# Optimization experiments

Hardware: AMD Instinct MI355X
Metric: run time of the kernel (lower is better)

## Reference

```python
import jax, jax.numpy as jnp
import numpy as np

EPS = 1e-12
ATTEND_SCALE = 8.0

def _l2norm(t, axis=-1):
    n = jnp.sqrt(jnp.sum(t * t, axis=axis, keepdims=True))
    return t / jnp.maximum(n, EPS)

def setup_inputs() -> dict:
    key = jax.random.key(0)
    k1, k2, k3, k4 = jax.random.split(key, 4)
    b, n, dim = 4, 8192, 1024
    heads, dim_head = 16, 64
    dim_inner = heads * dim_head
    x = jax.random.normal(k1, (b, n, dim), dtype=jnp.float32)
    gamma = jnp.ones((dim,), dtype=jnp.float32)  # RMSNorm gamma
    # torch Linear(dim, 3*dim_inner, bias=False): store as [dim, 3*dim_inner] for x @ W
    w_qkv = jax.random.normal(k2, (dim, 3 * dim_inner), dtype=jnp.float32) * (dim ** -0.5)
    temperature = jnp.zeros((heads, 1, 1), dtype=jnp.float32)
    w_out = jax.random.normal(k3, (dim_inner, dim), dtype=jnp.float32) * (dim_inner ** -0.5)
    return {"x": x, "gamma": gamma, "w_qkv": w_qkv, "temperature": temperature, "w_out": w_out}

def reference(x, gamma, w_qkv, temperature, w_out):
    b, n, dim = x.shape
    heads = temperature.shape[0]
    dim_head = w_qkv.shape[1] // (3 * heads)
    # RMSNorm: F.normalize(x, dim=-1) * sqrt(dim) * gamma
    xn = _l2norm(x) * (dim ** 0.5) * gamma
    qkv = xn @ w_qkv  # [b, n, 3*h*d]
    qkv = qkv.reshape(b, n, 3, heads, dim_head).transpose(2, 0, 3, 4, 1)  # [3, b, h, d, n]
    q, k, v = qkv[0], qkv[1], qkv[2]
    orig_v = v
    # l2-normalize q, k over the sequence axis (last dim of [b,h,d,n])
    q = _l2norm(q) * jnp.exp(temperature)  # temperature [h,1,1] broadcasts
    k = _l2norm(k)
    # attention over the feature axis: sim [b, h, d, d]
    sim = jnp.einsum('bhdn,bhen->bhde', q, k) * ATTEND_SCALE
    attn = jax.nn.softmax(sim, axis=-1)
    out = jnp.einsum('bhde,bhen->bhdn', attn, v)  # [b, h, d, n]
    out = out.transpose(0, 3, 1, 2).reshape(b, n, heads * dim_head) @ w_out  # [b, n, dim]
    return out, orig_v
```

## Files before the change

### kernel.cpp

```cpp
#include <hip/hip_runtime.h>
#include <hip/hip_bf16.h>

#define DEVI __device__ __forceinline__

using bf16x8 = __attribute__((ext_vector_type(8))) __bf16;
using f32x4  = __attribute__((ext_vector_type(4))) float;
using u16x8  = __attribute__((ext_vector_type(8))) unsigned short;

DEVI unsigned short f2bf(float f) {
  unsigned int u = __float_as_uint(f);
  u = (u + 0x7FFFu + ((u >> 16) & 1u)) >> 16;
  return (unsigned short)u;
}
DEVI float bf2f(unsigned short s) { return __uint_as_float(((unsigned int)s) << 16); }

DEVI void gld_lds16(const unsigned short* g, unsigned short* l) {
  __builtin_amdgcn_global_load_lds(
      (const __attribute__((address_space(1))) void*)g,
      (__attribute__((address_space(3))) void*)l, 16, 0, 0);
}

__global__ __launch_bounds__(256) void transpose_cast_kernel(const float* __restrict__ in,
                                                             unsigned short* __restrict__ out,
                                                             int R, int C) {
  __shared__ float tile[32][33];
  const int c0 = blockIdx.x * 32, r0 = blockIdx.y * 32;
  const int tx = threadIdx.x & 31, ty = threadIdx.x >> 5;
  for (int rr = ty; rr < 32; rr += 8)
    tile[rr][tx] = in[(size_t)(r0 + rr) * C + c0 + tx];
  __syncthreads();
  for (int cc = ty; cc < 32; cc += 8)
    out[(size_t)(c0 + cc) * R + r0 + tx] = f2bf(tile[tx][cc]);
}

__global__ __launch_bounds__(256) void castv_kernel(const float* __restrict__ w_qkv,
                                                    unsigned short* __restrict__ Wv_nt) {
  const int i = blockIdx.x * 256 + threadIdx.x;
  const int k = i >> 8, he4 = (i & 255) * 4;
  const float4 v = *(const float4*)&w_qkv[(size_t)k * 3072 + 2048 + he4];
  ushort4 o;
  o.x = f2bf(v.x); o.y = f2bf(v.y); o.z = f2bf(v.z); o.w = f2bf(v.w);
  *(ushort4*)&Wv_nt[(size_t)k * 1024 + he4] = o;
}

__global__ __launch_bounds__(256) void transpose_bf16x4_kernel(const unsigned short* __restrict__ in,
                                                               unsigned short* __restrict__ out) {
  __shared__ unsigned short tile[64][68];
  const int r0 = blockIdx.x * 64;
  const int c0 = blockIdx.y * 64;
  const int t = threadIdx.x;
  const int tr = t >> 4, tc4 = (t & 15) * 4;
#pragma unroll
  for (int p = 0; p < 4; ++p) {
    const int rr = p * 16 + tr;
    *(ushort4*)&tile[rr][tc4] = *(const ushort4*)&in[(size_t)(r0 + rr) * 1024 + c0 + tc4];
  }
  __syncthreads();
#pragma unroll
  for (int p = 0; p < 4; ++p) {
    const int cc = p * 16 + tr;
    ushort4 o;
    o.x = tile[tc4 + 0][cc];
    o.y = tile[tc4 + 1][cc];
    o.z = tile[tc4 + 2][cc];
    o.w = tile[tc4 + 3][cc];
    *(ushort4*)&out[(size_t)(c0 + cc) * 32768 + r0 + tc4] = o;
  }
}

__global__ __launch_bounds__(256) void rmsnorm_kernel(const float* __restrict__ x,
                                                      const float* __restrict__ gamma,
                                                      unsigned short* __restrict__ xn) {
  __shared__ float wsum[4];
  const int row = blockIdx.x;
  const int t = threadIdx.x;
  const float4 v = *(const float4*)&x[(size_t)row * 1024 + t * 4];
  float s = v.x * v.x + v.y * v.y + v.z * v.z + v.w * v.w;
  for (int off = 32; off; off >>= 1) s += __shfl_down(s, off);
  if ((t & 63) == 0) wsum[t >> 6] = s;
  __syncthreads();
  const float tot = wsum[0] + wsum[1] + wsum[2] + wsum[3];
  const float scale = 32.0f / fmaxf(sqrtf(tot), 1e-12f);
  const float4 g = *(const float4*)&gamma[t * 4];
  ushort4 o;
  o.x = f2bf(v.x * scale * g.x);
  o.y = f2bf(v.y * scale * g.y);
  o.z = f2bf(v.z * scale * g.z);
  o.w = f2bf(v.w * scale * g.w);
  *(ushort4*)&xn[(size_t)row * 1024 + t * 4] = o;
}

__global__ __launch_bounds__(256) void gemm_gram_kernel(const unsigned short* __restrict__ xnT,
                                                        unsigned short* __restrict__ Gp) {
  if (blockIdx.x > blockIdx.y) return;
  __shared__ __align__(16) unsigned short Al[4096];
  __shared__ __align__(16) unsigned short Bl[4096];
  const int tid = threadIdx.x;
  const int lane = tid & 63, wid = tid >> 6;
  const int wr = wid >> 1, wc = wid & 1;
  const int r = lane & 15, kg = lane >> 4;
  const int rw0 = tid >> 2, q0 = (tid & 3) * 8;
  const size_t row0 = (size_t)blockIdx.y * 128, col0 = (size_t)blockIdx.x * 128;
  const int z = blockIdx.z;
  const size_t koff = (size_t)(z >> 2) * 8192 + (size_t)(z & 3) * 2048;
  f32x4 acc[4][4] = {};
  for (int k0 = 0; k0 < 2048; k0 += 32) {
    __syncthreads();
    gld_lds16(&xnT[(row0 + rw0) * 32768 + koff + k0 + q0], &Al[tid * 8]);
    gld_lds16(&xnT[(row0 + rw0 + 64) * 32768 + koff + k0 + q0], &Al[2048 + tid * 8]);
    gld_lds16(&xnT[(col0 + rw0) * 32768 + koff + k0 + q0], &Bl[tid * 8]);
    gld_lds16(&xnT[(col0 + rw0 + 64) * 32768 + koff + k0 + q0], &Bl[2048 + tid * 8]);
    __syncthreads();
    bf16x8 af[4], bfr[4];
#pragma unroll
    for (int m = 0; m < 4; ++m) af[m] = *(const bf16x8*)&Al[(wr * 64 + m * 16 + r) * 32 + kg * 8];
#pragma unroll
    for (int n = 0; n < 4; ++n) bfr[n] = *(const bf16x8*)&Bl[(wc * 64 + n * 16 + r) * 32 + kg * 8];
#pragma unroll
    for (int m = 0; m < 4; ++m)
#pragma unroll
      for (int n = 0; n < 4; ++n)
        acc[m][n] = __builtin_amdgcn_mfma_f32_16x16x32_bf16(af[m], bfr[n], acc[m][n], 0, 0, 0);
  }
  unsigned short* C = Gp + ((size_t)z << 20);
  const int rbase = wr * 64 + (lane >> 4) * 4;
  const int cbase = wc * 64 + (lane & 15);
#pragma unroll
  for (int m = 0; m < 4; ++m)
#pragma unroll
    for (int n = 0; n < 4; ++n)
#pragma unroll
      for (int j = 0; j < 4; ++j)
        C[(row0 + rbase + m * 16 + j) * 1024 + col0 + cbase + n * 16] = f2bf(acc[m][n][j]);
}

__global__ __launch_bounds__(256) void greduce_kernel(const unsigned short* __restrict__ Gp,
                                                      unsigned short* __restrict__ G) {
  const int tj = blockIdx.x, ti = blockIdx.y, b = blockIdx.z;
  if ((tj >> 1) > (ti >> 1)) return;
  __shared__ float lds[64][65];
  const int t = threadIdx.x;
  const int r = t >> 2, c0 = (t & 3) * 16;
  const size_t idx = (size_t)(ti * 64 + r) * 1024 + tj * 64 + c0;
  float v[16];
#pragma unroll
  for (int j = 0; j < 16; ++j) v[j] = 0.f;
  for (int s = 0; s < 4; ++s) {
    const unsigned short* p = Gp + ((size_t)(b * 4 + s) << 20) + idx;
#pragma unroll
    for (int j = 0; j < 16; ++j) v[j] += bf2f(p[j]);
  }
  unsigned short* Gb = G + ((size_t)b << 20);
  __attribute__((aligned(16))) unsigned short buf[16];
#pragma unroll
  for (int j = 0; j < 16; ++j) buf[j] = f2bf(v[j]);
  { int4* dst = (int4*)&Gb[idx]; const int4* src = (const int4*)buf; dst[0] = src[0]; dst[1] = src[1]; }
  if ((ti >> 1) != (tj >> 1)) {
#pragma unroll
    for (int j = 0; j < 16; ++j) lds[r][c0 + j] = v[j];
    __syncthreads();
    const int x = t >> 2, y0 = (t & 3) * 16;
#pragma unroll
    for (int j = 0; j < 16; ++j) buf[j] = f2bf(lds[y0 + j][x]);
    int4* dst = (int4*)&Gb[(size_t)(tj * 64 + x) * 1024 + ti * 64 + y0];
    const int4* src = (const int4*)buf;
    dst[0] = src[0]; dst[1] = src[1];
  }
}

__global__ __launch_bounds__(256) void gemm_bt_batch_bf16(const unsigned short* __restrict__ A,
                                                          const unsigned short* __restrict__ Bt,
                                                          unsigned short* __restrict__ C,
                                                          int N, int K,
                                                          long long aStr, long long bStr, long long cStr) {
  __shared__ __align__(16) unsigned short Al[4096];
  __shared__ __align__(16) unsigned short Bl[4096];
  A += (size_t)blockIdx.z * aStr; Bt += (size_t)blockIdx.z * bStr; C += (size_t)blockIdx.z * cStr;
  const int tid = threadIdx.x;
  const int lane = tid & 63, wid = tid >> 6;
  const int wr = wid >> 1, wc = wid & 1;
  const int r = lane & 15, kg = lane >> 4;
  const int rw0 = tid >> 2, q0 = (tid & 3) * 8;
  const size_t row0 = (size_t)blockIdx.y * 128, col0 = (size_t)blockIdx.x * 128;
  f32x4 acc[4][4] = {};
  for (int k0 = 0; k0 < K; k0 += 32) {
    __syncthreads();
    gld_lds16(&A[(row0 + rw0) * K + k0 + q0], &Al[tid * 8]);
    gld_lds16(&A[(row0 + rw0 + 64) * K + k0 + q0], &Al[2048 + tid * 8]);
    gld_lds16(&Bt[(col0 + rw0) * K + k0 + q0], &Bl[tid * 8]);
    gld_lds16(&Bt[(col0 + rw0 + 64) * K + k0 + q0], &Bl[2048 + tid * 8]);
    __syncthreads();
    bf16x8 af[4], bfr[4];
#pragma unroll
    for (int m = 0; m < 4; ++m) af[m] = *(const bf16x8*)&Al[(wr * 64 + m * 16 + r) * 32 + kg * 8];
#pragma unroll
    for (int n = 0; n < 4; ++n) bfr[n] = *(const bf16x8*)&Bl[(wc * 64 + n * 16 + r) * 32 + kg * 8];
#pragma unroll
    for (int m = 0; m < 4; ++m)
#pragma unroll
      for (int n = 0; n < 4; ++n)
        acc[m][n] = __builtin_amdgcn_mfma_f32_16x16x32_bf16(af[m], bfr[n], acc[m][n], 0, 0, 0);
  }
  const int rbase = wr * 64 + (lane >> 4) * 4;
  const int cbase = wc * 64 + (lane & 15);
#pragma unroll
  for (int m = 0; m < 4; ++m)
#pragma unroll
    for (int n = 0; n < 4; ++n)
#pragma unroll
      for (int j = 0; j < 4; ++j)
        C[(row0 + rbase + m * 16 + j) * N + col0 + cbase + n * 16] = f2bf(acc[m][n][j]);
}

DEVI void stage256(const unsigned short* __restrict__ gA,
                   const unsigned short* __restrict__ gB,
                   unsigned short* lA, unsigned short* lB,
                   int k0, int w, int lane) {
  const int dr = lane >> 3;
  const int ks = (lane & 7) ^ dr;
  const size_t lo = (size_t)dr * 1024 + k0 + ks * 8;
#pragma unroll
  for (int i = 0; i < 4; ++i) {
    const int oct = w * 4 + i;
    gld_lds16(gA + (size_t)oct * 8192 + lo, lA + oct * 512 + lane * 8);
    gld_lds16(gB + (size_t)oct * 8192 + lo, lB + oct * 512 + lane * 8);
  }
}

DEVI void compute256(const unsigned short* __restrict__ lA,
                     const unsigned short* __restrict__ lB,
                     int wm, int wn, int lane, f32x4 (&acc)[8][4]) {
  const int r = lane & 15, kg = lane >> 4;
  const int r7 = r & 7;
#pragma unroll
  for (int ksl = 0; ksl < 2; ++ksl) {
    const int sA = (((ksl << 2) + kg) ^ r7) * 8;
    bf16x8 af[8], bfr[4];
#pragma unroll
    for (int m = 0; m < 8; ++m)
      af[m] = *(const bf16x8*)&lA[(wm * 128 + m * 16 + r) * 64 + sA];
#pragma unroll
    for (int n = 0; n < 4; ++n)
      bfr[n] = *(const bf16x8*)&lB[(wn * 64 + n * 16 + r) * 64 + sA];
#pragma unroll
    for (int m = 0; m < 8; ++m)
#pragma unroll
      for (int n = 0; n < 4; ++n)
        acc[m][n] = __builtin_amdgcn_mfma_f32_16x16x32_bf16(af[m], bfr[n], acc[m][n], 0, 0, 0);
  }
}

#define VOUT_BAR()  __builtin_amdgcn_sched_barrier(0); __builtin_amdgcn_s_barrier(); \
                    __builtin_amdgcn_sched_barrier(0)
#define VOUT_W8()   asm volatile("s_waitcnt vmcnt(8)" ::: "memory")
#define VOUT_W0()   asm volatile("s_waitcnt vmcnt(0)" ::: "memory")

__global__ __launch_bounds__(512, 2) void gemm_vout256_kernel(
    const unsigned short* __restrict__ A,
    const unsigned short* __restrict__ BtV,
    const unsigned short* __restrict__ WfoldT,
    float* __restrict__ origv,
    float* __restrict__ outp) {
  __shared__ __align__(16) unsigned short Al[2][16384];
  __shared__ __align__(16) unsigned short Bl[2][16384];
  const int tid = threadIdx.x;
  const int lane = tid & 63;
  const int w = tid >> 6;
  const int wm = w >> 2, wn = w & 3;
  const int cb = blockIdx.x & 7;
  const int rb = blockIdx.x >> 3;
  const int b = rb >> 5;
  const unsigned short* gA = A + (size_t)rb * 256 * 1024;
  const unsigned short* gB = (cb < 4)
      ? BtV + (size_t)cb * 256 * 1024
      : WfoldT + ((size_t)b << 20) + (size_t)(cb - 4) * 256 * 1024;

  f32x4 acc[8][4] = {};
  stage256(gA, gB, Al[0], Bl[0], 0, w, lane);
#pragma unroll 1
  for (int tt = 0; tt < 7; ++tt) {
    stage256(gA, gB, Al[1], Bl[1], (tt * 2 + 1) * 64, w, lane);
    VOUT_W8(); VOUT_BAR();
    __builtin_amdgcn_s_setprio(1);
    compute256(Al[0], Bl[0], wm, wn, lane, acc);
    __builtin_amdgcn_s_setprio(0);
    VOUT_BAR();
    stage256(gA, gB, Al[0], Bl[0], (tt * 2 + 2) * 64, w, lane);
    VOUT_W8(); VOUT_BAR();
    __builtin_amdgcn_s_setprio(1);
    compute256(Al[1], Bl[1], wm, wn, lane, acc);
    __builtin_amdgcn_s_setprio(0);
    VOUT_BAR();
  }
  stage256(gA, gB, Al[1], Bl[1], 15 * 64, w, lane);
  VOUT_W8(); VOUT_BAR();
  __builtin_amdgcn_s_setprio(1);
  compute256(Al[0], Bl[0], wm, wn, lane, acc);
  __builtin_amdgcn_s_setprio(0);
  VOUT_BAR();
  VOUT_W0(); VOUT_BAR();
  __builtin_amdgcn_s_setprio(1);
  compute256(Al[1], Bl[1], wm, wn, lane, acc);
  __builtin_amdgcn_s_setprio(0);

  const int rr = (lane >> 4) * 4;
  const int cc = lane & 15;
  if (cb < 4) {
    const int nbase = (rb & 31) * 256 + wm * 128;
#pragma unroll
    for (int m = 0; m < 8; ++m)
#pragma unroll
      for (int n = 0; n < 4; ++n) {
        const int hd = cb * 256 + wn * 64 + n * 16 + cc;
        const float4 o4 = make_float4(acc[m][n][0], acc[m][n][1], acc[m][n][2], acc[m][n][3]);
        *(float4*)&origv[((size_t)b * 1024 + hd) * 8192 + nbase + m * 16 + rr] = o4;
      }
  } else {
    const size_t grow0 = (size_t)rb * 256 + wm * 128;
    const int gc0 = (cb - 4) * 256 + wn * 64;
#pragma unroll
    for (int m = 0; m < 8; ++m)
#pragma unroll
      for (int n = 0; n < 4; ++n)
#pragma unroll
        for (int j = 0; j < 4; ++j)
          outp[(grow0 + m * 16 + rr + j) * 1024 + gc0 + n * 16 + cc] = acc[m][n][j];
  }
}

__global__ __launch_bounds__(256) void norms_kernel(const unsigned short* __restrict__ UTt,
                                                    const unsigned short* __restrict__ wqkvT,
                                                    float* __restrict__ qkn2) {
  const int t = threadIdx.x;
  const int rloc = t >> 4, lane16 = t & 15;
  const int row = blockIdx.x * 16 + rloc;
  const int b = row >> 11, r2 = row & 2047;
  const unsigned short* pa = UTt + ((size_t)b << 21) + (size_t)r2 * 1024 + lane16 * 64;
  const unsigned short* pb = wqkvT + (size_t)r2 * 1024 + lane16 * 64;
  float s = 0.f;
  for (int i = 0; i < 64; i += 8) {
    const u16x8 va = *(const u16x8*)&pa[i];
    const u16x8 vb = *(const u16x8*)&pb[i];
#pragma unroll
    for (int j = 0; j < 8; ++j) s += bf2f(va[j]) * bf2f(vb[j]);
  }
  for (int off = 8; off; off >>= 1) s += __shfl_down(s, off, 16);
  if (lane16 == 0) qkn2[row] = s;
}

__global__ __launch_bounds__(256) void sim_softmax_kernel(const unsigned short* __restrict__ wqkvT,
                                                          const unsigned short* __restrict__ UTt,
                                                          const float* __restrict__ qkn2,
                                                          const float* __restrict__ temperature,
                                                          float* __restrict__ attn) {
  __shared__ __align__(16) unsigned short Aql[64 * 128];
  __shared__ __align__(16) unsigned short Bkl[64 * 128];
  __shared__ float qknl[2][64];
  const int bh = blockIdx.x;
  const int b = bh >> 4, h = bh & 15;
  const int t = threadIdx.x;
  const int lane = t & 63, w = t >> 6;
  const unsigned short* UTtb = UTt + ((size_t)b << 21);
  if (t < 128) {
    const int sel = t >> 6, dd = t & 63;
    qknl[sel][dd] = fmaxf(sqrtf(qkn2[b * 2048 + sel * 1024 + h * 64 + dd]), 1e-12f);
  }
  const unsigned short* AqG = UTtb + (size_t)(h * 64) * 1024;
  const unsigned short* BkG = wqkvT + (size_t)(1024 + h * 64) * 1024;
  const int r = lane & 15, kg = lane >> 4;
  const int srow = t >> 4, scol = (t & 15) * 8;
  f32x4 acc[4] = {};
  for (int k0 = 0; k0 < 1024; k0 += 128) {
    __syncthreads();
#pragma unroll
    for (int c = 0; c < 4; ++c) {
      gld_lds16(&AqG[(size_t)(c * 16 + srow) * 1024 + k0 + scol], &Aql[c * 2048 + t * 8]);
      gld_lds16(&BkG[(size_t)(c * 16 + srow) * 1024 + k0 + scol], &Bkl[c * 2048 + t * 8]);
    }
    __syncthreads();
#pragma unroll
    for (int kk = 0; kk < 128; kk += 32) {
      const bf16x8 af = *(const bf16x8*)&Aql[(w * 16 + r) * 128 + kk + kg * 8];
#pragma unroll
      for (int n = 0; n < 4; ++n) {
        const bf16x8 bfr = *(const bf16x8*)&Bkl[(n * 16 + r) * 128 + kk + kg * 8];
        acc[n] = __builtin_amdgcn_mfma_f32_16x16x32_bf16(af, bfr, acc[n], 0, 0, 0);
      }
    }
  }
  const float sc = 8.f * __expf(temperature[h]);
  const int colq = lane & 15, rq = lane >> 4;
#pragma unroll
  for (int j = 0; j < 4; ++j) {
    const int d = w * 16 + rq * 4 + j;
    const float qd = qknl[0][d];
    float sv[4];
#pragma unroll
    for (int n = 0; n < 4; ++n) sv[n] = acc[n][j] * sc / (qd * qknl[1][n * 16 + colq]);
    float mj = fmaxf(fmaxf(sv[0], sv[1]), fmaxf(sv[2], sv[3]));
    for (int msk = 1; msk < 16; msk <<= 1) mj = fmaxf(mj, __shfl_xor(mj, msk));
    float p[4], sum = 0.f;
#pragma unroll
    for (int n = 0; n < 4; ++n) { p[n] = __expf(sv[n] - mj); sum += p[n]; }
    for (int msk = 1; msk < 16; msk <<= 1) sum += __shfl_xor(sum, msk);
    const float inv = 1.f / sum;
#pragma unroll
    for (int n = 0; n < 4; ++n)
      attn[(size_t)bh * 4096 + d * 64 + n * 16 + colq] = p[n] * inv;
  }
}

__global__ __launch_bounds__(256) void w2t_kernel(const float* __restrict__ attn,
                                                  const float* __restrict__ w_out,
                                                  unsigned short* __restrict__ W2T) {
  __shared__ float al[64][64];
  __shared__ float wl[64][64];
  const int bh = blockIdx.y;
  const int b = bh >> 4, h = bh & 15;
  const int c0 = blockIdx.x * 256;
  const int t = threadIdx.x, e = t & 63, g = t >> 6;
  const int dr = t >> 2, q4 = (t & 3) * 16;
#pragma unroll
  for (int j = 0; j < 16; j += 4)
    *(float4*)&al[dr][q4 + j] = *(const float4*)&attn[(size_t)bh * 4096 + dr * 64 + q4 + j];
  for (int cbk = 0; cbk < 4; ++cbk) {
    __syncthreads();
#pragma unroll
    for (int j = 0; j < 16; j += 4)
      *(float4*)&wl[dr][q4 + j] = *(const float4*)&w_out[(size_t)(h * 64 + dr) * 1024 + c0 + cbk * 64 + q4 + j];
    __syncthreads();
#pragma unroll
    for (int i = 0; i < 16; ++i) {
      const int cc = g * 16 + i;
      float s = 0.f;
#pragma unroll 8
      for (int d = 0; d < 64; ++d) s += al[d][e] * wl[d][cc];
      W2T[((size_t)b << 20) + (size_t)(c0 + cbk * 64 + cc) * 1024 + h * 64 + e] = f2bf(s);
    }
  }
}

extern "C" void kernel_launch(void* const* d_in, const int* in_sizes, int n_in,
                              void* d_out, int out_size, void* d_ws, size_t ws_size,
                              hipStream_t stream) {
  const float* x     = (const float*)d_in[0];
  const float* gamma = (const float*)d_in[1];
  const float* w_qkv = (const float*)d_in[2];
  const float* temp  = (const float*)d_in[3];
  const float* w_out = (const float*)d_in[4];
  char* ws = (char*)d_ws;
  unsigned short* wqkvT  = (unsigned short*)(ws);
  unsigned short* Wv_nt  = (unsigned short*)(ws + 6291456);
  unsigned short* xn     = (unsigned short*)(ws + 8388608);
  unsigned short* xnT    = (unsigned short*)(ws + 75497472);
  unsigned short* Gp     = (unsigned short*)(ws + 142606336);
  unsigned short* G      = (unsigned short*)(ws + 176160768);
  unsigned short* UTt    = (unsigned short*)(ws + 184549376);
  float* qkn2            = (float*)(ws + 201326592);
  float* attn            = (float*)(ws + 201359360);
  unsigned short* W2T    = (unsigned short*)(ws + 202407936);
  unsigned short* WfoldT = (unsigned short*)(ws + 210796544);
  float* outp  = (float*)d_out;
  float* origv = outp + (size_t)33554432;

  transpose_cast_kernel<<<dim3(96, 32), 256, 0, stream>>>(w_qkv, wqkvT, 1024, 3072);
  castv_kernel<<<1024, 256, 0, stream>>>(w_qkv, Wv_nt);
  rmsnorm_kernel<<<32768, 256, 0, stream>>>(x, gamma, xn);
  transpose_bf16x4_kernel<<<dim3(512, 16), 256, 0, stream>>>(xn, xnT);
  gemm_gram_kernel<<<dim3(8, 8, 16), 256, 0, stream>>>(xnT, Gp);
  greduce_kernel<<<dim3(16, 16, 4), 256, 0, stream>>>(Gp, G);
  gemm_bt_batch_bf16<<<dim3(8, 16, 4), 256, 0, stream>>>(wqkvT, G, UTt, 1024, 1024,
                                                         0LL, 1LL << 20, 1LL << 21);
  norms_kernel<<<512, 256, 0, stream>>>(UTt, wqkvT, qkn2);
  sim_softmax_kernel<<<64, 256, 0, stream>>>(wqkvT, UTt, qkn2, temp, attn);
  w2t_kernel<<<dim3(4, 64), 256, 0, stream>>>(attn, w_out, W2T);
  gemm_bt_batch_bf16<<<dim3(8, 8, 4), 256, 0, stream>>>(W2T, Wv_nt, WfoldT, 1024, 1024,
                                                        1LL << 20, 0LL, 1LL << 20);
  gemm_vout256_kernel<<<1024, 512, 0, stream>>>(xn, wqkvT + (size_t)2048 * 1024, WfoldT,
                                                origv, outp);
}
```

Measured before the change: 510.8 us.

## Restructure vout GEMM into 4-slot K=32 pipeline with three slices in flight

Replaces the double-buffered K=64 staging in the fused V/out GEMM with a 4-slot ring of K=32 slices, keeping three global-to-LDS loads in flight while one slice is computed. The LDS swizzle changes to match the narrower 32-element rows, and the barriers drop the compiler sched_barrier fences in favour of plain asm s_barrier. The aim is to hide more global-load latency behind the MFMAs. In exchange it needs twice as many barriers per K step, gives the compiler less to schedule per barrier, and the swizzle has only four positions, which may cause more LDS bank conflicts.

```diff
diff --git a/kernel.cpp b/kernel.cpp
--- a/kernel.cpp
+++ b/kernel.cpp
@@ -212,48 +212,48 @@
         C[(row0 + rbase + m * 16 + j) * N + col0 + cbase + n * 16] = f2bf(acc[m][n][j]);
 }
 
-DEVI void stage256(const unsigned short* __restrict__ gA,
-                   const unsigned short* __restrict__ gB,
-                   unsigned short* lA, unsigned short* lB,
-                   int k0, int w, int lane) {
-  const int dr = lane >> 3;
-  const int ks = (lane & 7) ^ dr;
-  const size_t lo = (size_t)dr * 1024 + k0 + ks * 8;
-#pragma unroll
-  for (int i = 0; i < 4; ++i) {
-    const int oct = w * 4 + i;
-    gld_lds16(gA + (size_t)oct * 8192 + lo, lA + oct * 512 + lane * 8);
-    gld_lds16(gB + (size_t)oct * 8192 + lo, lB + oct * 512 + lane * 8);
-  }
-}
-
-DEVI void compute256(const unsigned short* __restrict__ lA,
-                     const unsigned short* __restrict__ lB,
-                     int wm, int wn, int lane, f32x4 (&acc)[8][4]) {
+DEVI void stage_slice(const unsigned short* __restrict__ gA,
+                      const unsigned short* __restrict__ gB,
+                      unsigned short* lA, unsigned short* lB,
+                      int s, int slot, int w, int lane) {
+  const int ric = lane >> 2;
+  const int phys = lane & 3;
+  const int kg = phys ^ (ric & 3);
+#pragma unroll
+  for (int i = 0; i < 2; ++i) {
+    const int c = w * 2 + i;
+    const int row = c * 16 + ric;
+    const size_t goff = (size_t)row * 1024 + s * 32 + kg * 8;
+    gld_lds16(gA + goff, lA + slot * 8192 + c * 512 + lane * 8);
+    gld_lds16(gB + goff, lB + slot * 8192 + c * 512 + lane * 8);
+  }
+}
+
+DEVI void compute_slice(const unsigned short* lA, const unsigned short* lB,
+                        int slot, int wm, int wn, int lane, f32x4 (&acc)[8][4]) {
   const int r = lane & 15, kg = lane >> 4;
-  const int r7 = r & 7;
-#pragma unroll
-  for (int ksl = 0; ksl < 2; ++ksl) {
-    const int sA = (((ksl << 2) + kg) ^ r7) * 8;
-    bf16x8 af[8], bfr[4];
-#pragma unroll
-    for (int m = 0; m < 8; ++m)
-      af[m] = *(const bf16x8*)&lA[(wm * 128 + m * 16 + r) * 64 + sA];
+  const int sA = (kg ^ (r & 3)) * 8;
+  const unsigned short* pA = lA + slot * 8192 + (wm * 128 + r) * 32 + sA;
+  const unsigned short* pB = lB + slot * 8192 + (wn * 64 + r) * 32 + sA;
+  bf16x8 af[8], bfr[4];
+#pragma unroll
+  for (int m = 0; m < 8; ++m) af[m] = *(const bf16x8*)(pA + m * 512);
+#pragma unroll
+  for (int n = 0; n < 4; ++n) bfr[n] = *(const bf16x8*)(pB + n * 512);
+  __builtin_amdgcn_s_setprio(1);
+#pragma unroll
+  for (int m = 0; m < 8; ++m)
 #pragma unroll
     for (int n = 0; n < 4; ++n)
-      bfr[n] = *(const bf16x8*)&lB[(wn * 64 + n * 16 + r) * 64 + sA];
-#pragma unroll
-    for (int m = 0; m < 8; ++m)
-#pragma unroll
-      for (int n = 0; n < 4; ++n)
-        acc[m][n] = __builtin_amdgcn_mfma_f32_16x16x32_bf16(af[m], bfr[n], acc[m][n], 0, 0, 0);
-  }
-}
-
-#define VOUT_BAR()  __builtin_amdgcn_sched_barrier(0); __builtin_amdgcn_s_barrier(); \
-                    __builtin_amdgcn_sched_barrier(0)
-#define VOUT_W8()   asm volatile("s_waitcnt vmcnt(8)" ::: "memory")
-#define VOUT_W0()   asm volatile("s_waitcnt vmcnt(0)" ::: "memory")
+      acc[m][n] = __builtin_amdgcn_mfma_f32_16x16x32_bf16(af[m], bfr[n], acc[m][n], 0, 0, 0);
+  __builtin_amdgcn_s_setprio(0);
+}
+
+#define VBAR()  asm volatile("s_barrier" ::: "memory")
+#define VW12()  asm volatile("s_waitcnt vmcnt(12)" ::: "memory")
+#define VW8()   asm volatile("s_waitcnt vmcnt(8)" ::: "memory")
+#define VW4()   asm volatile("s_waitcnt vmcnt(4)" ::: "memory")
+#define VW0()   asm volatile("s_waitcnt vmcnt(0)" ::: "memory")
 
 __global__ __launch_bounds__(512, 2) void gemm_vout256_kernel(
     const unsigned short* __restrict__ A,
@@ -261,8 +261,8 @@
     const unsigned short* __restrict__ WfoldT,
     float* __restrict__ origv,
     float* __restrict__ outp) {
-  __shared__ __align__(16) unsigned short Al[2][16384];
-  __shared__ __align__(16) unsigned short Bl[2][16384];
+  __shared__ __align__(16) unsigned short lA[4 * 8192];
+  __shared__ __align__(16) unsigned short lB[4 * 8192];
   const int tid = threadIdx.x;
   const int lane = tid & 63;
   const int w = tid >> 6;
@@ -276,32 +276,25 @@
       : WfoldT + ((size_t)b << 20) + (size_t)(cb - 4) * 256 * 1024;
 
   f32x4 acc[8][4] = {};
-  stage256(gA, gB, Al[0], Bl[0], 0, w, lane);
+  stage_slice(gA, gB, lA, lB, 0, 0, w, lane);
+  stage_slice(gA, gB, lA, lB, 1, 1, w, lane);
+  stage_slice(gA, gB, lA, lB, 2, 2, w, lane);
 #pragma unroll 1
-  for (int tt = 0; tt < 7; ++tt) {
-    stage256(gA, gB, Al[1], Bl[1], (tt * 2 + 1) * 64, w, lane);
-    VOUT_W8(); VOUT_BAR();
-    __builtin_amdgcn_s_setprio(1);
-    compute256(Al[0], Bl[0], wm, wn, lane, acc);
-    __builtin_amdgcn_s_setprio(0);
-    VOUT_BAR();
-    stage256(gA, gB, Al[0], Bl[0], (tt * 2 + 2) * 64, w, lane);
-    VOUT_W8(); VOUT_BAR();
-    __builtin_amdgcn_s_setprio(1);
-    compute256(Al[1], Bl[1], wm, wn, lane, acc);
-    __builtin_amdgcn_s_setprio(0);
-    VOUT_BAR();
-  }
-  stage256(gA, gB, Al[1], Bl[1], 15 * 64, w, lane);
-  VOUT_W8(); VOUT_BAR();
-  __builtin_amdgcn_s_setprio(1);
-  compute256(Al[0], Bl[0], wm, wn, lane, acc);
-  __builtin_amdgcn_s_setprio(0);
-  VOUT_BAR();
-  VOUT_W0(); VOUT_BAR();
-  __builtin_amdgcn_s_setprio(1);
-  compute256(Al[1], Bl[1], wm, wn, lane, acc);
-  __builtin_amdgcn_s_setprio(0);
+  for (int t4 = 0; t4 < 7; ++t4) {
+    const int sb = t4 * 4;
+#pragma unroll
+    for (int j = 0; j < 4; ++j) {
+      stage_slice(gA, gB, lA, lB, sb + j + 3, (j + 3) & 3, w, lane);
+      VW12(); VBAR();
+      compute_slice(lA, lB, j, wm, wn, lane, acc);
+      VBAR();
+    }
+  }
+  stage_slice(gA, gB, lA, lB, 31, 3, w, lane);
+  VW12(); VBAR(); compute_slice(lA, lB, 0, wm, wn, lane, acc); VBAR();
+  VW8();  VBAR(); compute_slice(lA, lB, 1, wm, wn, lane, acc); VBAR();
+  VW4();  VBAR(); compute_slice(lA, lB, 2, wm, wn, lane, acc); VBAR();
+  VW0();  VBAR(); compute_slice(lA, lB, 3, wm, wn, lane, acc);
 
   const int rr = (lane >> 4) * 4;
   const int cc = lane & 15;
```

Result: slower. 523.3 us (+2.4%).

## Use 256x256 double-buffered MFMA tiles for the Gram GEMM

Applied to the files above, without the earlier changes.

Replaces the 128x128 single-buffered Gram kernel with a 512-thread, 256x256-tile kernel. It reuses the swizzled, double-buffered global-to-LDS staging and compute helpers from the vout GEMM, with their staging stride now a parameter. The aim is higher data reuse per LDS load and overlap of loads with MFMA work. The reduction kernel's lower-triangle tile test is adjusted to the coarser block granularity. The catch is fewer blocks (4x4 triangle x16, so 160 active) on a large GPU, which may underfill the compute units.

```diff
diff --git a/kernel.cpp b/kernel.cpp
--- a/kernel.cpp
+++ b/kernel.cpp
@@ -90,54 +90,109 @@
   *(ushort4*)&xn[(size_t)row * 1024 + t * 4] = o;
 }
 
-__global__ __launch_bounds__(256) void gemm_gram_kernel(const unsigned short* __restrict__ xnT,
-                                                        unsigned short* __restrict__ Gp) {
+DEVI void stage256(const unsigned short* __restrict__ gA,
+                   const unsigned short* __restrict__ gB,
+                   unsigned short* lA, unsigned short* lB,
+                   int k0, int w, int lane, size_t gstride) {
+  const int dr = lane >> 3;
+  const int ks = (lane & 7) ^ dr;
+  const size_t lo = (size_t)dr * gstride + k0 + ks * 8;
+#pragma unroll
+  for (int i = 0; i < 4; ++i) {
+    const int oct = w * 4 + i;
+    gld_lds16(gA + (size_t)oct * 8 * gstride + lo, lA + oct * 512 + lane * 8);
+    gld_lds16(gB + (size_t)oct * 8 * gstride + lo, lB + oct * 512 + lane * 8);
+  }
+}
+
+DEVI void compute256(const unsigned short* __restrict__ lA,
+                     const unsigned short* __restrict__ lB,
+                     int wm, int wn, int lane, f32x4 (&acc)[8][4]) {
+  const int r = lane & 15, kg = lane >> 4;
+  const int r7 = r & 7;
+#pragma unroll
+  for (int ksl = 0; ksl < 2; ++ksl) {
+    const int sA = (((ksl << 2) + kg) ^ r7) * 8;
+    bf16x8 af[8], bfr[4];
+#pragma unroll
+    for (int m = 0; m < 8; ++m)
+      af[m] = *(const bf16x8*)&lA[(wm * 128 + m * 16 + r) * 64 + sA];
+#pragma unroll
+    for (int n = 0; n < 4; ++n)
+      bfr[n] = *(const bf16x8*)&lB[(wn * 64 + n * 16 + r) * 64 + sA];
+#pragma unroll
+    for (int m = 0; m < 8; ++m)
+#pragma unroll
+      for (int n = 0; n < 4; ++n)
+        acc[m][n] = __builtin_amdgcn_mfma_f32_16x16x32_bf16(af[m], bfr[n], acc[m][n], 0, 0, 0);
+  }
+}
+
+#define VOUT_BAR()  __builtin_amdgcn_sched_barrier(0); __builtin_amdgcn_s_barrier(); \
+                    __builtin_amdgcn_sched_barrier(0)
+#define VOUT_W8()   asm volatile("s_waitcnt vmcnt(8)" ::: "memory")
+#define VOUT_W0()   asm volatile("s_waitcnt vmcnt(0)" ::: "memory")
+
+__global__ __launch_bounds__(512, 2) void gemm_gram256_kernel(
+    const unsigned short* __restrict__ xnT, unsigned short* __restrict__ Gp) {
   if (blockIdx.x > blockIdx.y) return;
-  __shared__ __align__(16) unsigned short Al[4096];
-  __shared__ __align__(16) unsigned short Bl[4096];
+  __shared__ __align__(16) unsigned short Al[2][16384];
+  __shared__ __align__(16) unsigned short Bl[2][16384];
   const int tid = threadIdx.x;
-  const int lane = tid & 63, wid = tid >> 6;
-  const int wr = wid >> 1, wc = wid & 1;
-  const int r = lane & 15, kg = lane >> 4;
-  const int rw0 = tid >> 2, q0 = (tid & 3) * 8;
-  const size_t row0 = (size_t)blockIdx.y * 128, col0 = (size_t)blockIdx.x * 128;
+  const int lane = tid & 63;
+  const int w = tid >> 6;
+  const int wm = w >> 2, wn = w & 3;
   const int z = blockIdx.z;
   const size_t koff = (size_t)(z >> 2) * 8192 + (size_t)(z & 3) * 2048;
-  f32x4 acc[4][4] = {};
-  for (int k0 = 0; k0 < 2048; k0 += 32) {
-    __syncthreads();
-    gld_lds16(&xnT[(row0 + rw0) * 32768 + koff + k0 + q0], &Al[tid * 8]);
-    gld_lds16(&xnT[(row0 + rw0 + 64) * 32768 + koff + k0 + q0], &Al[2048 + tid * 8]);
-    gld_lds16(&xnT[(col0 + rw0) * 32768 + koff + k0 + q0], &Bl[tid * 8]);
-    gld_lds16(&xnT[(col0 + rw0 + 64) * 32768 + koff + k0 + q0], &Bl[2048 + tid * 8]);
-    __syncthreads();
-    bf16x8 af[4], bfr[4];
-#pragma unroll
-    for (int m = 0; m < 4; ++m) af[m] = *(const bf16x8*)&Al[(wr * 64 + m * 16 + r) * 32 + kg * 8];
-#pragma unroll
-    for (int n = 0; n < 4; ++n) bfr[n] = *(const bf16x8*)&Bl[(wc * 64 + n * 16 + r) * 32 + kg * 8];
-#pragma unroll
-    for (int m = 0; m < 4; ++m)
-#pragma unroll
-      for (int n = 0; n < 4; ++n)
-        acc[m][n] = __builtin_amdgcn_mfma_f32_16x16x32_bf16(af[m], bfr[n], acc[m][n], 0, 0, 0);
-  }
+  const unsigned short* gA = xnT + (size_t)blockIdx.y * 256 * 32768 + koff;
+  const unsigned short* gB = xnT + (size_t)blockIdx.x * 256 * 32768 + koff;
+
+  f32x4 acc[8][4] = {};
+  stage256(gA, gB, Al[0], Bl[0], 0, w, lane, 32768);
+#pragma unroll 1
+  for (int tt = 0; tt < 15; ++tt) {
+    stage256(gA, gB, Al[1], Bl[1], (tt * 2 + 1) * 64, w, lane, 32768);
+    VOUT_W8(); VOUT_BAR();
+    __builtin_amdgcn_s_setprio(1);
+    compute256(Al[0], Bl[0], wm, wn, lane, acc);
+    __builtin_amdgcn_s_setprio(0);
+    VOUT_BAR();
+    stage256(gA, gB, Al[0], Bl[0], (tt * 2 + 2) * 64, w, lane, 32768);
+    VOUT_W8(); VOUT_BAR();
+    __builtin_amdgcn_s_setprio(1);
+    compute256(Al[1], Bl[1], wm, wn, lane, acc);
+    __builtin_amdgcn_s_setprio(0);
+    VOUT_BAR();
+  }
+  stage256(gA, gB, Al[1], Bl[1], 31 * 64, w, lane, 32768);
+  VOUT_W8(); VOUT_BAR();
+  __builtin_amdgcn_s_setprio(1);
+  compute256(Al[0], Bl[0], wm, wn, lane, acc);
+  __builtin_amdgcn_s_setprio(0);
+  VOUT_BAR();
+  VOUT_W0(); VOUT_BAR();
+  __builtin_amdgcn_s_setprio(1);
+  compute256(Al[1], Bl[1], wm, wn, lane, acc);
+  __builtin_amdgcn_s_setprio(0);
+
   unsigned short* C = Gp + ((size_t)z << 20);
-  const int rbase = wr * 64 + (lane >> 4) * 4;
-  const int cbase = wc * 64 + (lane & 15);
-#pragma unroll
-  for (int m = 0; m < 4; ++m)
+  const int rr = (lane >> 4) * 4;
+  const int cc = lane & 15;
+  const size_t grow0 = (size_t)blockIdx.y * 256 + wm * 128;
+  const int gc0 = blockIdx.x * 256 + wn * 64;
+#pragma unroll
+  for (int m = 0; m < 8; ++m)
 #pragma unroll
     for (int n = 0; n < 4; ++n)
 #pragma unroll
       for (int j = 0; j < 4; ++j)
-        C[(row0 + rbase + m * 16 + j) * 1024 + col0 + cbase + n * 16] = f2bf(acc[m][n][j]);
+        C[(grow0 + m * 16 + rr + j) * 1024 + gc0 + n * 16 + cc] = f2bf(acc[m][n][j]);
 }
 
 __global__ __launch_bounds__(256) void greduce_kernel(const unsigned short* __restrict__ Gp,
                                                       unsigned short* __restrict__ G) {
   const int tj = blockIdx.x, ti = blockIdx.y, b = blockIdx.z;
-  if ((tj >> 1) > (ti >> 1)) return;
+  if ((tj >> 2) > (ti >> 2)) return;
   __shared__ float lds[64][65];
   const int t = threadIdx.x;
   const int r = t >> 2, c0 = (t & 3) * 16;
@@ -155,7 +210,7 @@
 #pragma unroll
   for (int j = 0; j < 16; ++j) buf[j] = f2bf(v[j]);
   { int4* dst = (int4*)&Gb[idx]; const int4* src = (const int4*)buf; dst[0] = src[0]; dst[1] = src[1]; }
-  if ((ti >> 1) != (tj >> 1)) {
+  if ((ti >> 2) != (tj >> 2)) {
 #pragma unroll
     for (int j = 0; j < 16; ++j) lds[r][c0 + j] = v[j];
     __syncthreads();
@@ -211,49 +266,6 @@
       for (int j = 0; j < 4; ++j)
         C[(row0 + rbase + m * 16 + j) * N + col0 + cbase + n * 16] = f2bf(acc[m][n][j]);
 }
-
-DEVI void stage256(const unsigned short* __restrict__ gA,
-                   const unsigned short* __restrict__ gB,
-                   unsigned short* lA, unsigned short* lB,
-                   int k0, int w, int lane) {
-  const int dr = lane >> 3;
-  const int ks = (lane & 7) ^ dr;
-  const size_t lo = (size_t)dr * 1024 + k0 + ks * 8;
-#pragma unroll
-  for (int i = 0; i < 4; ++i) {
-    const int oct = w * 4 + i;
-    gld_lds16(gA + (size_t)oct * 8192 + lo, lA + oct * 512 + lane * 8);
-    gld_lds16(gB + (size_t)oct * 8192 + lo, lB + oct * 512 + lane * 8);
-  }
-}
-
-DEVI void compute256(const unsigned short* __restrict__ lA,
-                     const unsigned short* __restrict__ lB,
-                     int wm, int wn, int lane, f32x4 (&acc)[8][4]) {
-  const int r = lane & 15, kg = lane >> 4;
-  const int r7 = r & 7;
-#pragma unroll
-  for (int ksl = 0; ksl < 2; ++ksl) {
-    const int sA = (((ksl << 2) + kg) ^ r7) * 8;
-    bf16x8 af[8], bfr[4];
-#pragma unroll
-    for (int m = 0; m < 8; ++m)
-      af[m] = *(const bf16x8*)&lA[(wm * 128 + m * 16 + r) * 64 + sA];
-#pragma unroll
-    for (int n = 0; n < 4; ++n)
-      bfr[n] = *(const bf16x8*)&lB[(wn * 64 + n * 16 + r) * 64 + sA];
-#pragma unroll
-    for (int m = 0; m < 8; ++m)
-#pragma unroll
-      for (int n = 0; n < 4; ++n)
-        acc[m][n] = __builtin_amdgcn_mfma_f32_16x16x32_bf16(af[m], bfr[n], acc[m][n], 0, 0, 0);
-  }
-}
-
-#define VOUT_BAR()  __builtin_amdgcn_sched_barrier(0); __builtin_amdgcn_s_barrier(); \
-                    __builtin_amdgcn_sched_barrier(0)
-#define VOUT_W8()   asm volatile("s_waitcnt vmcnt(8)" ::: "memory")
-#define VOUT_W0()   asm volatile("s_waitcnt vmcnt(0)" ::: "memory")
 
 __global__ __launch_bounds__(512, 2) void gemm_vout256_kernel(
     const unsigned short* __restrict__ A,
@@ -276,23 +288,23 @@
       : WfoldT + ((size_t)b << 20) + (size_t)(cb - 4) * 256 * 1024;
 
   f32x4 acc[8][4] = {};
-  stage256(gA, gB, Al[0], Bl[0], 0, w, lane);
+  stage256(gA, gB, Al[0], Bl[0], 0, w, lane, 1024);
 #pragma unroll 1
   for (int tt = 0; tt < 7; ++tt) {
-    stage256(gA, gB, Al[1], Bl[1], (tt * 2 + 1) * 64, w, lane);
+    stage256(gA, gB, Al[1], Bl[1], (tt * 2 + 1) * 64, w, lane, 1024);
     VOUT_W8(); VOUT_BAR();
     __builtin_amdgcn_s_setprio(1);
     compute256(Al[0], Bl[0], wm, wn, lane, acc);
     __builtin_amdgcn_s_setprio(0);
     VOUT_BAR();
-    stage256(gA, gB, Al[0], Bl[0], (tt * 2 + 2) * 64, w, lane);
+    stage256(gA, gB, Al[0], Bl[0], (tt * 2 + 2) * 64, w, lane, 1024);
     VOUT_W8(); VOUT_BAR();
     __builtin_amdgcn_s_setprio(1);
     compute256(Al[1], Bl[1], wm, wn, lane, acc);
     __builtin_amdgcn_s_setprio(0);
     VOUT_BAR();
   }
-  stage256(gA, gB, Al[1], Bl[1], 15 * 64, w, lane);
+  stage256(gA, gB, Al[1], Bl[1], 15 * 64, w, lane, 1024);
   VOUT_W8(); VOUT_BAR();
   __builtin_amdgcn_s_setprio(1);
   compute256(Al[0], Bl[0], wm, wn, lane, acc);
@@ -467,7 +479,7 @@
   castv_kernel<<<1024, 256, 0, stream>>>(w_qkv, Wv_nt);
   rmsnorm_kernel<<<32768, 256, 0, stream>>>(x, gamma, xn);
   transpose_bf16x4_kernel<<<dim3(512, 16), 256, 0, stream>>>(xn, xnT);
-  gemm_gram_kernel<<<dim3(8, 8, 16), 256, 0, stream>>>(xnT, Gp);
+  gemm_gram256_kernel<<<dim3(4, 4, 16), 512, 0, stream>>>(xnT, Gp);
   greduce_kernel<<<dim3(16, 16, 4), 256, 0, stream>>>(Gp, G);
   gemm_bt_batch_bf16<<<dim3(8, 16, 4), 256, 0, stream>>>(wqkvT, G, UTt, 1024, 1024,
                                                          0LL, 1LL << 20, 1LL << 21);
```

After: 471.1 us. 1.08x faster.
